# Performance work log

Hardware: AMD Instinct MI355X
Metric: run time of the kernel (lower is better)

## Reference

```python
import jax, jax.numpy as jnp
import numpy as np

B, T, D_IN = 32, 128, 32
H1, H, PEN = 1024, 2048, 1024  # linear1 out, GRU hidden, penultimate
C, P = 64, 4                   # cultivars, phenos


def setup_inputs() -> dict:
    key = jax.random.key(0)
    ks = jax.random.split(key, 22)
    s = 0.02
    inp = {}
    inp['x'] = jax.random.normal(ks[0], (B, T, D_IN), dtype=jnp.float32)
    inp['cultivar_label'] = jax.random.randint(ks[1], (B, 1), 0, C)
    inp['W1'] = jax.random.normal(ks[2], (H1, D_IN), dtype=jnp.float32) * s
    inp['b1'] = jnp.zeros((H1,), jnp.float32)
    inp['W2'] = jax.random.normal(ks[3], (H, H1), dtype=jnp.float32) * s
    inp['b2'] = jnp.zeros((H,), jnp.float32)
    # GRU weights, PyTorch layout: gates stacked (r,z,n) along dim 0
    inp['W_ih'] = jax.random.normal(ks[4], (3 * H, H), dtype=jnp.float32) * s
    inp['b_ih'] = jnp.zeros((3 * H,), jnp.float32)
    inp['W_hh'] = jax.random.normal(ks[5], (3 * H, H), dtype=jnp.float32) * s
    inp['b_hh'] = jnp.zeros((3 * H,), jnp.float32)
    inp['W3'] = jax.random.normal(ks[6], (PEN, H), dtype=jnp.float32) * s
    inp['b3'] = jnp.zeros((PEN,), jnp.float32)
    # per-cultivar expert heads (each a Linear(PEN, 1)) packed as tables
    inp['W4'] = jax.random.normal(ks[7], (C, PEN), dtype=jnp.float32) * s
    inp['b4'] = jnp.zeros((C,), jnp.float32)
    inp['W5'] = jax.random.normal(ks[8], (C, PEN), dtype=jnp.float32) * s
    inp['b5'] = jnp.zeros((C,), jnp.float32)
    inp['W6'] = jax.random.normal(ks[9], (C, PEN), dtype=jnp.float32) * s
    inp['b6'] = jnp.zeros((C,), jnp.float32)
    inp['Wp'] = jax.random.normal(ks[10], (P, C, PEN), dtype=jnp.float32) * s
    inp['bp'] = jnp.zeros((P, C), jnp.float32)
    return inp


def _gru(x_seq, W_ih, b_ih, W_hh, b_hh):
    # x_seq: [B,T,H]; PyTorch GRU gate order (r, z, n)
    Bd, Hd = x_seq.shape[0], W_hh.shape[1]
    xp = jnp.einsum('bth,gh->btg', x_seq, W_ih) + b_ih  # [B,T,3H]

    def step(h, xp_t):
        hp = h @ W_hh.T + b_hh
        xr, xz, xn = jnp.split(xp_t, 3, axis=-1)
        hr, hz, hn = jnp.split(hp, 3, axis=-1)
        r = jax.nn.sigmoid(xr + hr)
        z = jax.nn.sigmoid(xz + hz)
        n = jnp.tanh(xn + r * hn)
        h_new = (1.0 - z) * n + z * h
        return h_new, h_new

    h0 = jnp.zeros((Bd, Hd), x_seq.dtype)
    _, hs = jax.lax.scan(step, h0, jnp.swapaxes(xp, 0, 1))  # [T,B,H]
    return jnp.swapaxes(hs, 0, 1)  # [B,T,H]


def reference(x, cultivar_label, W1, b1, W2, b2, W_ih, b_ih, W_hh, b_hh,
              W3, b3, W4, b4, W5, b5, W6, b6, Wp, bp):
    out = jax.nn.relu(jnp.einsum('btd,hd->bth', x, W1) + b1)
    out = jax.nn.relu(jnp.einsum('bth,gh->btg', out, W2) + b2)
    out = _gru(out, W_ih, b_ih, W_hh, b_hh)
    out_s = jax.nn.relu(jnp.einsum('bth,ph->btp', out, W3) + b3)  # [B,T,PEN]
    labels = cultivar_label[:, 0]

    def head(W, b):  # gather expert row per sample -> [B,T,1]
        return (jnp.einsum('btd,bd->bt', out_s, W[labels]) + b[labels][:, None])[..., None]

    out_lt_10 = head(W4, b4)
    out_lt_50 = head(W5, b5)
    out_lt_90 = head(W6, b6)
    # pheno heads: Wp[:, labels] -> [P,B,PEN]
    out_ph = jax.nn.sigmoid(
        jnp.einsum('btd,pbd->pbt', out_s, Wp[:, labels]) + bp[:, labels][:, :, None]
    )[..., None]  # [P,B,T,1]
    return (out_lt_10, out_lt_50, out_lt_90, out_ph, 0)
```

## Files before the change

kernel.cpp:

```cpp
#include <hip/hip_runtime.h>
#include <hip/hip_bf16.h>
#include <math.h>


typedef __bf16 bf16_t;
typedef __bf16 bf16x4 __attribute__((ext_vector_type(4)));
typedef __bf16 bf16x8 __attribute__((ext_vector_type(8)));
typedef float  f32x4  __attribute__((ext_vector_type(4)));
typedef int    i32x4  __attribute__((ext_vector_type(4)));
typedef unsigned int u32;

static __device__ __forceinline__ void zero4(f32x4& v) {
  v[0] = 0.0f; v[1] = 0.0f; v[2] = 0.0f; v[3] = 0.0f;
}

template <typename T>
static __device__ __forceinline__ bf16x8 load8_as_bf16(const T* p);
template <>
__device__ __forceinline__ bf16x8 load8_as_bf16<bf16_t>(const bf16_t* p) {
  return *(const bf16x8*)p;
}
template <>
__device__ __forceinline__ bf16x8 load8_as_bf16<float>(const float* p) {
  bf16x8 v;
#pragma unroll
  for (int u = 0; u < 8; ++u) v[u] = (bf16_t)p[u];
  return v;
}

static __device__ __forceinline__ void gload16(const bf16_t* g, bf16_t* l) {
  __builtin_amdgcn_global_load_lds(
      (const __attribute__((address_space(1))) u32*)g,
      (__attribute__((address_space(3))) u32*)l, 16, 0, 0);
}

__global__ __launch_bounds__(256) void cvt_f32_bf16(
    const float* __restrict__ s, bf16_t* __restrict__ d, int n8)
{
  const int i = blockIdx.x * 256 + threadIdx.x;
  if (i < n8) {
    const float* p = s + (size_t)i * 8;
    bf16x8 v;
#pragma unroll
    for (int u = 0; u < 8; ++u) v[u] = (bf16_t)p[u];
    *(bf16x8*)(d + (size_t)i * 8) = v;
  }
}

template <typename TA, typename TB>
__global__ __launch_bounds__(256) void gemm_bt(
    const TA* __restrict__ A, const TB* __restrict__ Bm,
    const float* __restrict__ bias, bf16_t* __restrict__ C,
    int M, int N, int K, int relu)
{
  __shared__ __align__(16) bf16_t As[128 * 32];
  __shared__ __align__(16) bf16_t Bs[128 * 32];

  const int tid  = threadIdx.x;
  const int lane = tid & 63;
  const int wave = tid >> 6;
  const int q    = lane >> 4;
  const int l15  = lane & 15;
  const int wr   = wave >> 1;
  const int wc   = wave & 1;
  const int m0   = blockIdx.y * 128;
  const int n0   = blockIdx.x * 128;

  f32x4 acc[4][4];
#pragma unroll
  for (int i = 0; i < 4; ++i)
#pragma unroll
    for (int j = 0; j < 4; ++j) zero4(acc[i][j]);

  const int se = wave * 512 + lane * 8;

  const int kt_count = K >> 5;
  for (int kt = 0; kt < kt_count; ++kt) {
    const int k0 = kt << 5;

    bf16x8 av[2], bv[2];
#pragma unroll
    for (int c = 0; c < 2; ++c) {
      const int e   = c * 2048 + se;
      const int row = e >> 5;
      const int col = e & 31;
      av[c] = load8_as_bf16<TA>(&A [(size_t)(m0 + row) * K + k0 + col]);
      bv[c] = load8_as_bf16<TB>(&Bm[(size_t)(n0 + row) * K + k0 + col]);
    }

    __syncthreads();
#pragma unroll
    for (int c = 0; c < 2; ++c) {
      *(bf16x8*)&As[c * 2048 + se] = av[c];
      *(bf16x8*)&Bs[c * 2048 + se] = bv[c];
    }
    __syncthreads();

    bf16x8 af[4], bfv[4];
#pragma unroll
    for (int i = 0; i < 4; ++i)
      af[i] = *(const bf16x8*)&As[(wr * 64 + i * 16 + l15) * 32 + q * 8];
#pragma unroll
    for (int j = 0; j < 4; ++j)
      bfv[j] = *(const bf16x8*)&Bs[(wc * 64 + j * 16 + l15) * 32 + q * 8];

#pragma unroll
    for (int i = 0; i < 4; ++i)
#pragma unroll
      for (int j = 0; j < 4; ++j)
        acc[i][j] = __builtin_amdgcn_mfma_f32_16x16x32_bf16(af[i], bfv[j], acc[i][j], 0, 0, 0);
  }

#pragma unroll
  for (int j = 0; j < 4; ++j) {
    const int n = n0 + wc * 64 + j * 16 + l15;
    const float bvl = bias[n];
#pragma unroll
    for (int i = 0; i < 4; ++i) {
      const int mbase = m0 + wr * 64 + i * 16 + q * 4;
#pragma unroll
      for (int r = 0; r < 4; ++r) {
        float v = acc[i][j][r] + bvl;
        if (relu) v = v > 0.0f ? v : 0.0f;
        C[(size_t)(mbase + r) * N + n] = (bf16_t)v;
      }
    }
  }
}

__global__ __launch_bounds__(256) void gemm_lds(
    const bf16_t* __restrict__ A, const bf16_t* __restrict__ Bm,
    const float* __restrict__ bias, bf16_t* __restrict__ C,
    int M, int N, int K, int relu)
{
  __shared__ __align__(16) bf16_t As[128 * 32];
  __shared__ __align__(16) bf16_t Bs[128 * 32];

  const int tid  = threadIdx.x;
  const int lane = tid & 63;
  const int wave = tid >> 6;
  const int q    = lane >> 4;
  const int l15  = lane & 15;
  const int wr   = wave >> 1;
  const int wc   = wave & 1;
  const int m0   = blockIdx.y * 128;
  const int n0   = blockIdx.x * 128;

  f32x4 acc[4][4];
#pragma unroll
  for (int i = 0; i < 4; ++i)
#pragma unroll
    for (int j = 0; j < 4; ++j) zero4(acc[i][j]);

  const int sew = wave * 512;
  const int se  = sew + lane * 8;

  const int kt_count = K >> 5;
  for (int kt = 0; kt < kt_count; ++kt) {
    const int k0 = kt << 5;

    __syncthreads();
#pragma unroll
    for (int c = 0; c < 2; ++c) {
      const int e   = c * 2048 + se;
      const int row = e >> 5;
      const int col = e & 31;
      gload16(&A [(size_t)(m0 + row) * K + k0 + col], &As[c * 2048 + sew]);
      gload16(&Bm[(size_t)(n0 + row) * K + k0 + col], &Bs[c * 2048 + sew]);
    }
    asm volatile("s_waitcnt vmcnt(0)" ::: "memory");
    __syncthreads();

    bf16x8 af[4], bfv[4];
#pragma unroll
    for (int i = 0; i < 4; ++i)
      af[i] = *(const bf16x8*)&As[(wr * 64 + i * 16 + l15) * 32 + q * 8];
#pragma unroll
    for (int j = 0; j < 4; ++j)
      bfv[j] = *(const bf16x8*)&Bs[(wc * 64 + j * 16 + l15) * 32 + q * 8];

#pragma unroll
    for (int i = 0; i < 4; ++i)
#pragma unroll
      for (int j = 0; j < 4; ++j)
        acc[i][j] = __builtin_amdgcn_mfma_f32_16x16x32_bf16(af[i], bfv[j], acc[i][j], 0, 0, 0);
  }

#pragma unroll
  for (int j = 0; j < 4; ++j) {
    const int n = n0 + wc * 64 + j * 16 + l15;
    const float bvl = bias[n];
#pragma unroll
    for (int i = 0; i < 4; ++i) {
      const int mbase = m0 + wr * 64 + i * 16 + q * 4;
#pragma unroll
      for (int r = 0; r < 4; ++r) {
        float v = acc[i][j][r] + bvl;
        if (relu) v = v > 0.0f ? v : 0.0f;
        C[(size_t)(mbase + r) * N + n] = (bf16_t)v;
      }
    }
  }
}

#define WROW 2056
#define NCOPY 8

__global__ __launch_bounds__(512, 2) void gru_persistent(
    const float* __restrict__ W_hh, const float* __restrict__ b_hh,
    const bf16_t* __restrict__ xp, bf16_t* __restrict__ hs,
    unsigned* __restrict__ arr,
    const float* __restrict__ W3, const float* __restrict__ b3,
    bf16_t* __restrict__ out_s)
{
  __shared__ __align__(16) bf16_t Ws[24 * WROW];
  __shared__ __align__(16) bf16_t W3s[4 * WROW];
  __shared__ __align__(16) float hp_p[8][32][28];
  __shared__ __align__(16) float hp3[8][32][8];
  __shared__ __align__(16) unsigned short stage[32][8];

  const int tid  = threadIdx.x;
  const int lane = tid & 63;
  const int wave = tid >> 6;
  const int q    = lane >> 4;
  const int l15  = lane & 15;
  const int bid  = blockIdx.x;
  const int j0   = bid * 8;
  const int j0s  = bid * 4;
  const int k0w  = wave * 256;

  for (int m = 0; m < 24; ++m) {
    const int gate = m >> 3;
    const float* src = W_hh + (size_t)(gate * 2048 + j0 + (m & 7)) * 2048;
    const int c = tid * 4;
    bf16x4 v;
#pragma unroll
    for (int u = 0; u < 4; ++u) v[u] = (bf16_t)src[c + u];
    *(bf16x4*)&Ws[m * WROW + c] = v;
  }
  for (int m = 0; m < 4; ++m) {
    const float* src = W3 + (size_t)(j0s + m) * 2048;
    const int c = tid * 4;
    bf16x4 v;
#pragma unroll
    for (int u = 0; u < 4; ++u) v[u] = (bf16_t)src[c + u];
    *(bf16x4*)&W3s[m * WROW + c] = v;
  }

  const bool pw = tid < 256;
  const int b  = (tid >> 3) & 31;
  const int jj = tid & 7;
  const int jg = j0 + jj;
  float bh_r = 0.f, bh_z = 0.f, bh_n = 0.f;
  if (pw) {
    bh_r = b_hh[jg];
    bh_z = b_hh[2048 + jg];
    bh_n = b_hh[4096 + jg];
  }
  const bool sw = (tid >= 256) && (tid < 384);
  const int b3t = (tid - 256) >> 2;
  const int c3  = (tid - 256) & 3;
  float b3v = 0.f;
  if (sw) b3v = b3[j0s + c3];

  const bf16_t* arow0 = &Ws[(size_t)l15 * WROW + k0w];
  const bf16_t* arow1 = &Ws[(size_t)(16 + (l15 & 7)) * WROW + k0w];
  const bf16_t* arow3 = &W3s[(size_t)(l15 & 3) * WROW + k0w];

  float hcur = 0.0f;

  float xr_c = 0.f, xz_c = 0.f, xn_c = 0.f;
  if (pw) {
    xr_c = (float)xp[(size_t)(b * 128 + 0) * 6144 + jg];
    xz_c = (float)xp[(size_t)(b * 128 + 0) * 6144 + 2048 + jg];
    xn_c = (float)xp[(size_t)(b * 128 + 0) * 6144 + 4096 + jg];
  }

  __syncthreads();

  for (int t = 0; t < 128; ++t) {
    if (t > 0) {
      const int c = bid & 7;
      const unsigned long long* f64p =
          (const unsigned long long*)(arr + ((size_t)(t - 1) * NCOPY + c) * 256)
          + wave * 16;
      const unsigned long long tgt = 0x0000000100000001ull;
      int guard = 0;
      for (;;) {
        unsigned long long v = tgt;
        if (lane < 16)
          v = __hip_atomic_load(f64p + lane, __ATOMIC_RELAXED,
                                __HIP_MEMORY_SCOPE_AGENT);
        if (__all(v == tgt)) break;
        __builtin_amdgcn_s_sleep(1);
        if (++guard > (1 << 20)) break;
      }

      bf16x8 bfr[2][8];
#pragma unroll
      for (int ct = 0; ct < 2; ++ct) {
        const bf16_t* bp_ = hs + ((size_t)(ct * 16 + l15) * 128 + (t - 1)) * 2048
                               + k0w + q * 8;
#pragma unroll
        for (int win = 0; win < 8; ++win)
          bfr[ct][win] = *(const bf16x8*)(bp_ + win * 32);
      }

      f32x4 acc[2][2];
#pragma unroll
      for (int rt = 0; rt < 2; ++rt)
#pragma unroll
        for (int ct = 0; ct < 2; ++ct) zero4(acc[rt][ct]);

#pragma unroll
      for (int win = 0; win < 8; ++win) {
        const bf16x8 a0 = *(const bf16x8*)(arow0 + win * 32 + q * 8);
        const bf16x8 a1 = *(const bf16x8*)(arow1 + win * 32 + q * 8);
        acc[0][0] = __builtin_amdgcn_mfma_f32_16x16x32_bf16(a0, bfr[0][win], acc[0][0], 0, 0, 0);
        acc[0][1] = __builtin_amdgcn_mfma_f32_16x16x32_bf16(a0, bfr[1][win], acc[0][1], 0, 0, 0);
        acc[1][0] = __builtin_amdgcn_mfma_f32_16x16x32_bf16(a1, bfr[0][win], acc[1][0], 0, 0, 0);
        acc[1][1] = __builtin_amdgcn_mfma_f32_16x16x32_bf16(a1, bfr[1][win], acc[1][1], 0, 0, 0);
      }

      f32x4 acc3[2];
      zero4(acc3[0]); zero4(acc3[1]);
#pragma unroll
      for (int win = 0; win < 8; ++win) {
        const bf16x8 a3 = *(const bf16x8*)(arow3 + win * 32 + q * 8);
        acc3[0] = __builtin_amdgcn_mfma_f32_16x16x32_bf16(a3, bfr[0][win], acc3[0], 0, 0, 0);
        acc3[1] = __builtin_amdgcn_mfma_f32_16x16x32_bf16(a3, bfr[1][win], acc3[1], 0, 0, 0);
      }

#pragma unroll
      for (int ct = 0; ct < 2; ++ct) {
        *(f32x4*)&hp_p[wave][ct * 16 + l15][q * 4] = acc[0][ct];
        if (q < 2)
          *(f32x4*)&hp_p[wave][ct * 16 + l15][16 + q * 4] = acc[1][ct];
      }
      if (q == 0) {
        *(f32x4*)&hp3[wave][l15][0]      = acc3[0];
        *(f32x4*)&hp3[wave][16 + l15][0] = acc3[1];
      }
    }
    __syncthreads();

    float xr_n = 0.f, xz_n = 0.f, xn_n = 0.f;
    if (pw) {
      float pr = 0.0f, pz = 0.0f, pn = 0.0f;
      if (t > 0) {
#pragma unroll
        for (int w = 0; w < 8; ++w) {
          pr += hp_p[w][b][jj];
          pz += hp_p[w][b][8 + jj];
          pn += hp_p[w][b][16 + jj];
        }
      }
      const float r_ = 1.0f / (1.0f + __expf(-(xr_c + pr + bh_r)));
      const float z_ = 1.0f / (1.0f + __expf(-(xz_c + pz + bh_z)));
      const float aa = xn_c + r_ * (pn + bh_n);
      const float et = __expf(-2.0f * aa);
      const float n_ = (1.0f - et) / (1.0f + et);
      hcur = (1.0f - z_) * n_ + z_ * hcur;

      if (t < 127) {
        const int tn = t + 1;
        xr_n = (float)xp[(size_t)(b * 128 + tn) * 6144 + jg];
        xz_n = (float)xp[(size_t)(b * 128 + tn) * 6144 + 2048 + jg];
        xn_n = (float)xp[(size_t)(b * 128 + tn) * 6144 + 4096 + jg];
      }

      union { bf16_t h; unsigned short u; } cv; cv.h = (bf16_t)hcur;
      stage[b][jj] = cv.u;
    } else if (sw && t > 0) {
      float s3 = 0.0f;
#pragma unroll
      for (int w = 0; w < 8; ++w) s3 += hp3[w][b3t][c3];
      s3 += b3v;
      if (s3 < 0.0f) s3 = 0.0f;
      out_s[((size_t)b3t * 128 + (t - 1)) * 1024 + j0s + c3] = (bf16_t)s3;
    }
    __syncthreads();

    if (wave == 0 && lane < 32) {
      const i32x4 val = *(const i32x4*)&stage[lane][0];
      bf16_t* dst = hs + ((size_t)lane * 128 + t) * 2048 + j0;
      asm volatile("global_store_dwordx4 %0, %1, off sc0 sc1"
                   :: "v"(dst), "v"(val) : "memory");
    }
    if (wave == 0) {
      asm volatile("s_waitcnt vmcnt(0)" ::: "memory");
      if (lane < NCOPY)
        __hip_atomic_store(arr + ((size_t)t * NCOPY + lane) * 256 + bid, 1u,
                           __ATOMIC_RELAXED, __HIP_MEMORY_SCOPE_AGENT);
    }
    if (t < 127) {
      xr_c = xr_n; xz_c = xz_n; xn_c = xn_n;
    }
  }

  {
    const int c = bid & 7;
    const unsigned long long* f64p =
        (const unsigned long long*)(arr + ((size_t)127 * NCOPY + c) * 256)
        + wave * 16;
    const unsigned long long tgt = 0x0000000100000001ull;
    int guard = 0;
    for (;;) {
      unsigned long long v = tgt;
      if (lane < 16)
        v = __hip_atomic_load(f64p + lane, __ATOMIC_RELAXED,
                              __HIP_MEMORY_SCOPE_AGENT);
      if (__all(v == tgt)) break;
      __builtin_amdgcn_s_sleep(1);
      if (++guard > (1 << 20)) break;
    }

    f32x4 acc3[2];
    zero4(acc3[0]); zero4(acc3[1]);
#pragma unroll
    for (int ct = 0; ct < 2; ++ct) {
      const bf16_t* bp_ = hs + ((size_t)(ct * 16 + l15) * 128 + 127) * 2048
                             + k0w + q * 8;
#pragma unroll
      for (int win = 0; win < 8; ++win) {
        const bf16x8 bv = *(const bf16x8*)(bp_ + win * 32);
        const bf16x8 a3 = *(const bf16x8*)(arow3 + win * 32 + q * 8);
        acc3[ct] = __builtin_amdgcn_mfma_f32_16x16x32_bf16(a3, bv, acc3[ct], 0, 0, 0);
      }
    }
    if (q == 0) {
      *(f32x4*)&hp3[wave][l15][0]      = acc3[0];
      *(f32x4*)&hp3[wave][16 + l15][0] = acc3[1];
    }
    __syncthreads();
    if (sw) {
      float s3 = 0.0f;
#pragma unroll
      for (int w = 0; w < 8; ++w) s3 += hp3[w][b3t][c3];
      s3 += b3v;
      if (s3 < 0.0f) s3 = 0.0f;
      out_s[((size_t)b3t * 128 + 127) * 1024 + j0s + c3] = (bf16_t)s3;
    }
  }
}

__global__ __launch_bounds__(256) void heads_kernel(
    const bf16_t* __restrict__ out_s, const int* __restrict__ labels,
    const float* __restrict__ W4, const float* __restrict__ b4,
    const float* __restrict__ W5, const float* __restrict__ b5,
    const float* __restrict__ W6, const float* __restrict__ b6,
    const float* __restrict__ Wp, const float* __restrict__ bp,
    float* __restrict__ out)
{
  const int bt  = blockIdx.x;
  const int b   = bt >> 7;
  const int lab = labels[b];
  const bf16_t* os  = out_s + (size_t)bt * 1024;
  const float* w4  = W4 + (size_t)lab * 1024;
  const float* w5  = W5 + (size_t)lab * 1024;
  const float* w6  = W6 + (size_t)lab * 1024;
  const float* wp0 = Wp + (size_t)lab * 1024;

  float s[7] = {0, 0, 0, 0, 0, 0, 0};
  for (int d = threadIdx.x; d < 1024; d += 256) {
    const float v = (float)os[d];
    s[0] += v * w4[d];
    s[1] += v * w5[d];
    s[2] += v * w6[d];
    s[3] += v * wp0[d];
    s[4] += v * wp0[65536 + d];
    s[5] += v * wp0[131072 + d];
    s[6] += v * wp0[196608 + d];
  }
#pragma unroll
  for (int i = 0; i < 7; ++i)
    for (int off = 32; off > 0; off >>= 1)
      s[i] += __shfl_down(s[i], off, 64);

  __shared__ float red[4][7];
  const int lane = threadIdx.x & 63, wave = threadIdx.x >> 6;
  if (lane == 0)
    for (int i = 0; i < 7; ++i) red[wave][i] = s[i];
  __syncthreads();
  if (threadIdx.x == 0) {
    float tsum[7];
    for (int i = 0; i < 7; ++i)
      tsum[i] = red[0][i] + red[1][i] + red[2][i] + red[3][i];
    out[bt]        = tsum[0] + b4[lab];
    out[4096 + bt] = tsum[1] + b5[lab];
    out[8192 + bt] = tsum[2] + b6[lab];
#pragma unroll
    for (int p = 0; p < 4; ++p) {
      const float v = tsum[3 + p] + bp[p * 64 + lab];
      out[12288 + p * 4096 + bt] = 1.0f / (1.0f + __expf(-v));
    }
  }
}

extern "C" void kernel_launch(void* const* d_in, const int* in_sizes, int n_in,
                              void* d_out, int out_size, void* d_ws, size_t ws_size,
                              hipStream_t stream)
{
  const float* x     = (const float*)d_in[0];
  const int*   label = (const int*)d_in[1];
  const float* W1    = (const float*)d_in[2];
  const float* b1    = (const float*)d_in[3];
  const float* W2    = (const float*)d_in[4];
  const float* b2    = (const float*)d_in[5];
  const float* W_ih  = (const float*)d_in[6];
  const float* b_ih  = (const float*)d_in[7];
  const float* W_hh  = (const float*)d_in[8];
  const float* b_hh  = (const float*)d_in[9];
  const float* W3    = (const float*)d_in[10];
  const float* b3    = (const float*)d_in[11];
  const float* W4    = (const float*)d_in[12];
  const float* b4    = (const float*)d_in[13];
  const float* W5    = (const float*)d_in[14];
  const float* b5    = (const float*)d_in[15];
  const float* W6    = (const float*)d_in[16];
  const float* b6    = (const float*)d_in[17];
  const float* Wp    = (const float*)d_in[18];
  const float* bp    = (const float*)d_in[19];

  char* ws = (char*)d_ws;
  bf16_t* W_ihb = (bf16_t*)(ws);
  bf16_t* out2  = (bf16_t*)(ws + (24u << 20));
  bf16_t* W2b   = (bf16_t*)(ws + (40u << 20));
  bf16_t* out1  = (bf16_t*)(ws + (44u << 20));
  bf16_t* xp    = (bf16_t*)(ws + (47u << 20));
  bf16_t* hs    = (bf16_t*)(ws);
  bf16_t* out_s = (bf16_t*)(ws + (16u << 20));
  unsigned* arr = (unsigned*)(ws + (95u << 20));
  float*  outp  = (float*)d_out;

  hipMemsetAsync(d_out, 0, (size_t)out_size * sizeof(float), stream);
  hipMemsetAsync(arr, 0, 1u << 20, stream);

  dim3 blk(256);
  cvt_f32_bf16<<<dim3(6144), blk, 0, stream>>>(W_ih, W_ihb, 1572864);
  cvt_f32_bf16<<<dim3(1024), blk, 0, stream>>>(W2, W2b, 262144);
  gemm_bt<float, float><<<dim3(8, 32), blk, 0, stream>>>(x, W1, b1, out1, 4096, 1024, 32, 1);
  gemm_lds<<<dim3(16, 32), blk, 0, stream>>>(out1, W2b, b2, out2, 4096, 2048, 1024, 1);
  gemm_lds<<<dim3(48, 32), blk, 0, stream>>>(out2, W_ihb, b_ih, xp, 4096, 6144, 2048, 0);
  {
    void* gru_args[] = { (void*)&W_hh, (void*)&b_hh, (void*)&xp, (void*)&hs,
                         (void*)&arr, (void*)&W3, (void*)&b3, (void*)&out_s };
    hipLaunchCooperativeKernel((void*)gru_persistent, dim3(256), dim3(512),
                               gru_args, 0, stream);
  }
  heads_kernel<<<dim3(4096), blk, 0, stream>>>(out_s, label, W4, b4, W5, b5, W6, b6, Wp, bp, outp);
}
```

Before: 1.274 ms.

## Fuse input-projection GEMM into persistent GRU kernel with ring buffer overlap

Removes the standalone xp = out2·W_ih GEMM and computes it inside the persistent GRU kernel. Each block produces tiles of xp into a 16-slot ring buffer, interleaved with the recurrent steps (4 K-chunks per step). A per-time-chunk counter signals when an xp tile is ready. The earlier GEMM outputs are permuted to time-major order so each xp tile covers whole timesteps. This targets overlap of the large input projection with the latency-bound recurrence. In exchange it adds extra synchronisation, a larger LDS scratch, and lowers occupancy to one block per CU.

```diff
diff --git a/kernel.cpp b/kernel.cpp
--- a/kernel.cpp
+++ b/kernel.cpp
@@ -9,6 +9,7 @@
 typedef float  f32x4  __attribute__((ext_vector_type(4)));
 typedef int    i32x4  __attribute__((ext_vector_type(4)));
 typedef unsigned int u32;
+typedef unsigned long long u64;
 
 static __device__ __forceinline__ void zero4(f32x4& v) {
   v[0] = 0.0f; v[1] = 0.0f; v[2] = 0.0f; v[3] = 0.0f;
@@ -51,7 +52,7 @@
 __global__ __launch_bounds__(256) void gemm_bt(
     const TA* __restrict__ A, const TB* __restrict__ Bm,
     const float* __restrict__ bias, bf16_t* __restrict__ C,
-    int M, int N, int K, int relu)
+    int M, int N, int K, int relu, int tmajor)
 {
   __shared__ __align__(16) bf16_t As[128 * 32];
   __shared__ __align__(16) bf16_t Bs[128 * 32];
@@ -122,7 +123,9 @@
       for (int r = 0; r < 4; ++r) {
         float v = acc[i][j][r] + bvl;
         if (relu) v = v > 0.0f ? v : 0.0f;
-        C[(size_t)(mbase + r) * N + n] = (bf16_t)v;
+        const int m = mbase + r;
+        const int pm = tmajor ? ((m & 127) * 32 + (m >> 7)) : m;
+        C[(size_t)pm * N + n] = (bf16_t)v;
       }
     }
   }
@@ -206,18 +209,142 @@
 #define WROW 2056
 #define NCOPY 8
 
-__global__ __launch_bounds__(512, 2) void gru_persistent(
+static __device__ __forceinline__ void produce_issue(
+    int c, int buf, int wg, int tid, int wave,
+    const bf16_t* out2t, const bf16_t* W_ihb, char* scr)
+{
+  const int tile_i = c >> 6;
+  const int id = wg + (tile_i << 8);
+  const int k0 = (c & 63) << 5;
+  bf16_t* dstA = (bf16_t*)(scr + buf * 16384);
+  bf16_t* dstB = dstA + 4096;
+  if (tid < 256) {
+    const int tc = id / 48;
+    const bf16_t* sb = out2t + (size_t)tc * 128 * 2048 + k0;
+    const int g0 = tid;
+    gload16(sb + (size_t)(g0 >> 2) * 2048 + (g0 & 3) * 8, dstA + (wave << 9));
+    const int g1 = tid + 256;
+    gload16(sb + (size_t)(g1 >> 2) * 2048 + (g1 & 3) * 8,
+            dstA + 2048 + (wave << 9));
+  } else {
+    const int nc = id % 48;
+    const int w4 = wave - 4;
+    const bf16_t* sb = W_ihb + (size_t)nc * 128 * 2048 + k0;
+    const int g0 = tid - 256;
+    gload16(sb + (size_t)(g0 >> 2) * 2048 + (g0 & 3) * 8, dstB + (w4 << 9));
+    const int g1 = g0 + 256;
+    gload16(sb + (size_t)(g1 >> 2) * 2048 + (g1 & 3) * 8,
+            dstB + 2048 + (w4 << 9));
+  }
+}
+
+static __device__ __forceinline__ void produce_mfma(
+    int buf, int wave, int q, int l15, char* scr, f32x4 (&pacc)[4][2])
+{
+  const bf16_t* pA = (const bf16_t*)(scr + buf * 16384);
+  const bf16_t* pB = pA + 4096;
+  const int wr = wave >> 2, wc = wave & 3;
+  bf16x8 af[4], bfv[2];
+#pragma unroll
+  for (int i = 0; i < 4; ++i)
+    af[i] = *(const bf16x8*)&pA[(wr * 64 + i * 16 + l15) * 32 + q * 8];
+#pragma unroll
+  for (int j = 0; j < 2; ++j)
+    bfv[j] = *(const bf16x8*)&pB[(wc * 32 + j * 16 + l15) * 32 + q * 8];
+#pragma unroll
+  for (int i = 0; i < 4; ++i)
+#pragma unroll
+    for (int j = 0; j < 2; ++j)
+      pacc[i][j] = __builtin_amdgcn_mfma_f32_16x16x32_bf16(af[i], bfv[j], pacc[i][j], 0, 0, 0);
+}
+
+static __device__ __forceinline__ void produce_epilogue(
+    int c, int wg, int tid, int wave, int q, int l15,
+    const float* b_ih, bf16_t* xpring, unsigned* tcnt, char* scr,
+    f32x4 (&pacc)[4][2])
+{
+  const int tile_i = c >> 6;
+  const int id = wg + (tile_i << 8);
+  const int tc = id / 48, nc = id % 48;
+  const int wr = wave >> 2, wc = wave & 3;
+  bf16_t* tld = (bf16_t*)scr;
+  float bv[2];
+#pragma unroll
+  for (int j = 0; j < 2; ++j) bv[j] = b_ih[nc * 128 + wc * 32 + j * 16 + l15];
+#pragma unroll
+  for (int half = 0; half < 2; ++half) {
+    __syncthreads();
+    if (wr == half) {
+#pragma unroll
+      for (int i = 0; i < 4; ++i)
+#pragma unroll
+        for (int j = 0; j < 2; ++j)
+#pragma unroll
+          for (int r = 0; r < 4; ++r)
+            tld[(i * 16 + q * 4 + r) * 128 + wc * 32 + j * 16 + l15] =
+                (bf16_t)(pacc[i][j][r] + bv[j]);
+    }
+    __syncthreads();
+    const int slotbase = (tc & 15) * 128 + half * 64;
+#pragma unroll
+    for (int s = 0; s < 2; ++s) {
+      const int g = tid * 2 + s;
+      const int row = g >> 4, col = (g & 15) << 3;
+      const i32x4 val = *(const i32x4*)&tld[row * 128 + col];
+      bf16_t* dst = xpring + (size_t)(slotbase + row) * 6144 + nc * 128 + col;
+      asm volatile("global_store_dwordx4 %0, %1, off sc0 sc1"
+                   :: "v"(dst), "v"(val) : "memory");
+    }
+  }
+  asm volatile("s_waitcnt vmcnt(0)" ::: "memory");
+  __syncthreads();
+  if (tid == 0)
+    __hip_atomic_fetch_add(tcnt + tc, 1u, __ATOMIC_RELAXED,
+                           __HIP_MEMORY_SCOPE_AGENT);
+#pragma unroll
+  for (int i = 0; i < 4; ++i) { zero4(pacc[i][0]); zero4(pacc[i][1]); }
+}
+
+static __device__ __forceinline__ void produce_run(
+    int c0, int n, int wg, int tid, int wave, int q, int l15,
+    const bf16_t* out2t, const bf16_t* W_ihb, const float* b_ih,
+    bf16_t* xpring, unsigned* tcnt, char* scr, f32x4 (&pacc)[4][2])
+{
+  asm volatile("s_waitcnt vmcnt(0)" ::: "memory");
+  produce_issue(c0, 0, wg, tid, wave, out2t, W_ihb, scr);
+  for (int s = 0; s < n; ++s) {
+    const int c = c0 + s;
+    if (s + 1 < n) {
+      produce_issue(c + 1, (s + 1) & 1, wg, tid, wave, out2t, W_ihb, scr);
+      asm volatile("s_waitcnt vmcnt(2)" ::: "memory");
+    } else {
+      asm volatile("s_waitcnt vmcnt(0)" ::: "memory");
+    }
+    __syncthreads();
+    produce_mfma(s & 1, wave, q, l15, scr, pacc);
+    __syncthreads();
+    if ((c & 63) == 63)
+      produce_epilogue(c, wg, tid, wave, q, l15, b_ih, xpring, tcnt, scr, pacc);
+  }
+}
+
+__global__ __launch_bounds__(512, 1) void gru_persistent(
     const float* __restrict__ W_hh, const float* __restrict__ b_hh,
-    const bf16_t* __restrict__ xp, bf16_t* __restrict__ hs,
-    unsigned* __restrict__ arr,
+    bf16_t* __restrict__ hs, unsigned* __restrict__ arr,
     const float* __restrict__ W3, const float* __restrict__ b3,
-    bf16_t* __restrict__ out_s)
+    bf16_t* __restrict__ out_s,
+    const bf16_t* __restrict__ out2t, const bf16_t* __restrict__ W_ihb,
+    const float* __restrict__ b_ih, bf16_t* __restrict__ xpring,
+    unsigned* __restrict__ tcnt)
 {
   __shared__ __align__(16) bf16_t Ws[24 * WROW];
   __shared__ __align__(16) bf16_t W3s[4 * WROW];
-  __shared__ __align__(16) float hp_p[8][32][28];
-  __shared__ __align__(16) float hp3[8][32][8];
-  __shared__ __align__(16) unsigned short stage[32][8];
+  __shared__ __align__(16) char scr[38912];
+
+  auto hp_p = (float (*)[32][28])(scr);
+  auto hp3  = (float (*)[32][8])(scr + 28672);
+  auto stg  = (unsigned short (*)[8])(scr + 36864);
+  auto xps  = (__bf16 (*)[3][8])(scr + 37376);
 
   const int tid  = threadIdx.x;
   const int lane = tid & 63;
@@ -225,6 +352,7 @@
   const int q    = lane >> 4;
   const int l15  = lane & 15;
   const int bid  = blockIdx.x;
+  const int wg   = bid;
   const int j0   = bid * 8;
   const int j0s  = bid * 4;
   const int k0w  = wave * 256;
@@ -263,39 +391,65 @@
   float b3v = 0.f;
   if (sw) b3v = b3[j0s + c3];
 
+  const int bb = tid / 6;
+  const int xg = (tid % 6) >> 1;
+  const int xh = tid & 1;
+
   const bf16_t* arow0 = &Ws[(size_t)l15 * WROW + k0w];
   const bf16_t* arow1 = &Ws[(size_t)(16 + (l15 & 7)) * WROW + k0w];
   const bf16_t* arow3 = &W3s[(size_t)(l15 & 3) * WROW + k0w];
 
+  f32x4 pacc[4][2];
+#pragma unroll
+  for (int i = 0; i < 4; ++i) { zero4(pacc[i][0]); zero4(pacc[i][1]); }
+
   float hcur = 0.0f;
 
-  float xr_c = 0.f, xz_c = 0.f, xn_c = 0.f;
-  if (pw) {
-    xr_c = (float)xp[(size_t)(b * 128 + 0) * 6144 + jg];
-    xz_c = (float)xp[(size_t)(b * 128 + 0) * 6144 + 2048 + jg];
-    xn_c = (float)xp[(size_t)(b * 128 + 0) * 6144 + 4096 + jg];
-  }
-
   __syncthreads();
 
+  produce_run(0, 64, wg, tid, wave, q, l15, out2t, W_ihb, b_ih,
+              xpring, tcnt, scr, pacc);
+
   for (int t = 0; t < 128; ++t) {
-    if (t > 0) {
-      const int c = bid & 7;
-      const unsigned long long* f64p =
-          (const unsigned long long*)(arr + ((size_t)(t - 1) * NCOPY + c) * 256)
-          + wave * 16;
-      const unsigned long long tgt = 0x0000000100000001ull;
+    if (t < 80) {
+      int c = 64 + 4 * t, left = 4;
+      while (left > 0) {
+        int n = 64 - (c & 63); if (n > left) n = left;
+        produce_run(c, n, wg, tid, wave, q, l15, out2t, W_ihb, b_ih,
+                    xpring, tcnt, scr, pacc);
+        c += n; left -= n;
+      }
+    }
+
+    {
+      const int tcn = t >> 2;
+      const u64 tgt = 0x0000000100000001ull;
+      const u64* f64p = (const u64*)(arr +
+          ((size_t)(t > 0 ? t - 1 : 0) * NCOPY + (bid & 7)) * 256) + wave * 16;
       int guard = 0;
       for (;;) {
-        unsigned long long v = tgt;
-        if (lane < 16)
+        u64 v = tgt; unsigned cc = 48;
+        if (t > 0 && lane < 16)
           v = __hip_atomic_load(f64p + lane, __ATOMIC_RELAXED,
                                 __HIP_MEMORY_SCOPE_AGENT);
-        if (__all(v == tgt)) break;
+        if (lane == 16)
+          cc = __hip_atomic_load(tcnt + tcn, __ATOMIC_RELAXED,
+                                 __HIP_MEMORY_SCOPE_AGENT);
+        if (__all(v == tgt && cc >= 48)) break;
         __builtin_amdgcn_s_sleep(1);
         if (++guard > (1 << 20)) break;
       }
-
+    }
+
+    u64 xv = 0;
+    if (tid < 192) {
+      const int slot = (t >> 2) & 15;
+      const size_t srow = (size_t)(slot * 128 + (t & 3) * 32 + bb);
+      const u64* src = (const u64*)(xpring + srow * 6144 + xg * 2048 + j0) + xh;
+      xv = __hip_atomic_load(src, __ATOMIC_RELAXED, __HIP_MEMORY_SCOPE_AGENT);
+    }
+
+    if (t > 0) {
       bf16x8 bfr[2][8];
 #pragma unroll
       for (int ct = 0; ct < 2; ++ct) {
@@ -342,9 +496,10 @@
         *(f32x4*)&hp3[wave][16 + l15][0] = acc3[1];
       }
     }
-    __syncthreads();
-
-    float xr_n = 0.f, xz_n = 0.f, xn_n = 0.f;
+    if (tid < 192)
+      ((u64*)&xps[bb][xg][0])[xh] = xv;
+    __syncthreads();
+
     if (pw) {
       float pr = 0.0f, pz = 0.0f, pn = 0.0f;
       if (t > 0) {
@@ -355,22 +510,18 @@
           pn += hp_p[w][b][16 + jj];
         }
       }
-      const float r_ = 1.0f / (1.0f + __expf(-(xr_c + pr + bh_r)));
-      const float z_ = 1.0f / (1.0f + __expf(-(xz_c + pz + bh_z)));
-      const float aa = xn_c + r_ * (pn + bh_n);
+      const float xr = (float)xps[b][0][jj];
+      const float xz = (float)xps[b][1][jj];
+      const float xn = (float)xps[b][2][jj];
+      const float r_ = 1.0f / (1.0f + __expf(-(xr + pr + bh_r)));
+      const float z_ = 1.0f / (1.0f + __expf(-(xz + pz + bh_z)));
+      const float aa = xn + r_ * (pn + bh_n);
       const float et = __expf(-2.0f * aa);
       const float n_ = (1.0f - et) / (1.0f + et);
       hcur = (1.0f - z_) * n_ + z_ * hcur;
 
-      if (t < 127) {
-        const int tn = t + 1;
-        xr_n = (float)xp[(size_t)(b * 128 + tn) * 6144 + jg];
-        xz_n = (float)xp[(size_t)(b * 128 + tn) * 6144 + 2048 + jg];
-        xn_n = (float)xp[(size_t)(b * 128 + tn) * 6144 + 4096 + jg];
-      }
-
       union { bf16_t h; unsigned short u; } cv; cv.h = (bf16_t)hcur;
-      stage[b][jj] = cv.u;
+      stg[b][jj] = cv.u;
     } else if (sw && t > 0) {
       float s3 = 0.0f;
 #pragma unroll
@@ -382,7 +533,7 @@
     __syncthreads();
 
     if (wave == 0 && lane < 32) {
-      const i32x4 val = *(const i32x4*)&stage[lane][0];
+      const i32x4 val = *(const i32x4*)&stg[lane][0];
       bf16_t* dst = hs + ((size_t)lane * 128 + t) * 2048 + j0;
       asm volatile("global_store_dwordx4 %0, %1, off sc0 sc1"
                    :: "v"(dst), "v"(val) : "memory");
@@ -393,20 +544,16 @@
         __hip_atomic_store(arr + ((size_t)t * NCOPY + lane) * 256 + bid, 1u,
                            __ATOMIC_RELAXED, __HIP_MEMORY_SCOPE_AGENT);
     }
-    if (t < 127) {
-      xr_c = xr_n; xz_c = xz_n; xn_c = xn_n;
-    }
   }
 
   {
     const int c = bid & 7;
-    const unsigned long long* f64p =
-        (const unsigned long long*)(arr + ((size_t)127 * NCOPY + c) * 256)
-        + wave * 16;
-    const unsigned long long tgt = 0x0000000100000001ull;
+    const u64* f64p =
+        (const u64*)(arr + ((size_t)127 * NCOPY + c) * 256) + wave * 16;
+    const u64 tgt = 0x0000000100000001ull;
     int guard = 0;
     for (;;) {
-      unsigned long long v = tgt;
+      u64 v = tgt;
       if (lane < 16)
         v = __hip_atomic_load(f64p + lane, __ATOMIC_RELAXED,
                               __HIP_MEMORY_SCOPE_AGENT);
@@ -428,6 +575,7 @@
         acc3[ct] = __builtin_amdgcn_mfma_f32_16x16x32_bf16(a3, bv, acc3[ct], 0, 0, 0);
       }
     }
+    __syncthreads();
     if (q == 0) {
       *(f32x4*)&hp3[wave][l15][0]      = acc3[0];
       *(f32x4*)&hp3[wave][16 + l15][0] = acc3[1];
@@ -523,28 +671,30 @@
   const float* bp    = (const float*)d_in[19];
 
   char* ws = (char*)d_ws;
-  bf16_t* W_ihb = (bf16_t*)(ws);
-  bf16_t* out2  = (bf16_t*)(ws + (24u << 20));
-  bf16_t* W2b   = (bf16_t*)(ws + (40u << 20));
-  bf16_t* out1  = (bf16_t*)(ws + (44u << 20));
-  bf16_t* xp    = (bf16_t*)(ws + (47u << 20));
-  bf16_t* hs    = (bf16_t*)(ws);
-  bf16_t* out_s = (bf16_t*)(ws + (16u << 20));
-  unsigned* arr = (unsigned*)(ws + (95u << 20));
-  float*  outp  = (float*)d_out;
+  bf16_t* W_ihb  = (bf16_t*)(ws);
+  bf16_t* out2t  = (bf16_t*)(ws + (24u << 20));
+  bf16_t* xpring = (bf16_t*)(ws + (40u << 20));
+  bf16_t* hs     = (bf16_t*)(ws + (64u << 20));
+  unsigned* arr  = (unsigned*)(ws + (80u << 20));
+  unsigned* tcnt = (unsigned*)(ws + (81u << 20));
+  bf16_t* out1t  = (bf16_t*)(ws + (84u << 20));
+  bf16_t* out_s  = (bf16_t*)(ws + (84u << 20));
+  bf16_t* W2b    = (bf16_t*)(ws + (92u << 20));
+  float*  outp   = (float*)d_out;
 
   hipMemsetAsync(d_out, 0, (size_t)out_size * sizeof(float), stream);
-  hipMemsetAsync(arr, 0, 1u << 20, stream);
+  hipMemsetAsync(ws + (80u << 20), 0, (1u << 20) + 4096, stream);
 
   dim3 blk(256);
   cvt_f32_bf16<<<dim3(6144), blk, 0, stream>>>(W_ih, W_ihb, 1572864);
   cvt_f32_bf16<<<dim3(1024), blk, 0, stream>>>(W2, W2b, 262144);
-  gemm_bt<float, float><<<dim3(8, 32), blk, 0, stream>>>(x, W1, b1, out1, 4096, 1024, 32, 1);
-  gemm_lds<<<dim3(16, 32), blk, 0, stream>>>(out1, W2b, b2, out2, 4096, 2048, 1024, 1);
-  gemm_lds<<<dim3(48, 32), blk, 0, stream>>>(out2, W_ihb, b_ih, xp, 4096, 6144, 2048, 0);
+  gemm_bt<float, float><<<dim3(8, 32), blk, 0, stream>>>(x, W1, b1, out1t, 4096, 1024, 32, 1, 1);
+  gemm_lds<<<dim3(16, 32), blk, 0, stream>>>(out1t, W2b, b2, out2t, 4096, 2048, 1024, 1);
   {
-    void* gru_args[] = { (void*)&W_hh, (void*)&b_hh, (void*)&xp, (void*)&hs,
-                         (void*)&arr, (void*)&W3, (void*)&b3, (void*)&out_s };
+    void* gru_args[] = { (void*)&W_hh, (void*)&b_hh, (void*)&hs, (void*)&arr,
+                         (void*)&W3, (void*)&b3, (void*)&out_s,
+                         (void*)&out2t, (void*)&W_ihb, (void*)&b_ih,
+                         (void*)&xpring, (void*)&tcnt };
     hipLaunchCooperativeKernel((void*)gru_persistent, dim3(256), dim3(512),
                                gru_args, 0, stream);
   }
```

Result: slower. 1.352 ms (+6.1%).
